# Optimization experiments

Hardware: AMD Instinct MI355X
Metric: run time of the kernel (lower is better)

## Reference

```python
import jax, jax.numpy as jnp
import numpy as np

QS_HIDDEN = 32


def quality_score(feat, W1, b1, W2, b2):
    # (h,5) -> (h,) per-qubit quality in [0,1]
    hdn = jax.nn.relu(feat @ W1 + b1)
    return jax.nn.sigmoid((hdn @ W2 + b2).squeeze(-1))


def _pair_cost(P_log, D, pairs):
    # mean over batch and pairs of sum_{p,q} P_ip * D_pq * P_jq
    Pi = P_log[:, pairs[:, 0], :]  # (batch, E, h)
    Pj = P_log[:, pairs[:, 1], :]  # (batch, E, h)
    return jnp.einsum('beh,hk,bek->be', Pi, D, Pj).mean()


def setup_inputs() -> dict:
    key = jax.random.key(0)
    ks = jax.random.split(key, 10)
    batch, h, L, E = 512, 256, 200, 512
    P = jax.random.uniform(ks[0], (batch, h, h), dtype=jnp.float32)
    P = P / P.sum(-1, keepdims=True)  # row-stochastic (stand-in for doubly stochastic)
    return {
        'P': P,
        'd_error': jax.random.uniform(ks[1], (h, h), dtype=jnp.float32),
        'd_hw': jax.random.uniform(ks[2], (h, h), dtype=jnp.float32),
        'hw_node_features': jax.random.uniform(ks[3], (h, 5), dtype=jnp.float32),
        'qubit_importance': jax.random.uniform(ks[4], (L,), dtype=jnp.float32),
        'W1': jax.random.normal(ks[5], (5, QS_HIDDEN), dtype=jnp.float32) * 0.5,
        'b1': jnp.zeros((QS_HIDDEN,), dtype=jnp.float32),
        'W2': jax.random.normal(ks[6], (QS_HIDDEN, 1), dtype=jnp.float32) * 0.5,
        'b2': jnp.zeros((1,), dtype=jnp.float32),
        'circuit_edge_pairs': jax.random.randint(ks[7], (E, 2), 0, L),
        'cross_circuit_pairs': jax.random.randint(ks[8], (E, 2), 0, L),
        'num_logical': L,
    }


def reference(P, d_error, d_hw, hw_node_features, qubit_importance, W1, b1, W2, b2,
              circuit_edge_pairs, cross_circuit_pairs, num_logical):
    alpha, lambda_sep = 0.3, 0.1
    P_log = P[:, :num_logical, :]  # (batch, L, h)

    # L_surr: error-aware edge loss
    l_surr = _pair_cost(P_log, d_error, circuit_edge_pairs)

    # L_node: node quality loss
    q = quality_score(hw_node_features, W1, b1, W2, b2)  # (h,)
    expected_quality = (P_log * q[None, None, :]).sum(-1)  # (batch, L)
    w_norm = qubit_importance / jnp.clip(qubit_importance.sum(), 1e-8)
    l_node = -(w_norm[None, :] * expected_quality).sum(-1).mean()

    # L_sep: separation loss with max-normalized hardware distance
    d_hw_norm = d_hw / jnp.clip(d_hw.max(), 1e-8)
    l_sep = -_pair_cost(P_log, d_hw_norm, cross_circuit_pairs)

    total = l_surr + alpha * l_node + lambda_sep * l_sep
    return total, l_surr, l_node, l_sep
```

## Files before the change

### kernel.cpp

```cpp
#include <hip/hip_runtime.h>


typedef __attribute__((ext_vector_type(8))) short short8;
typedef __attribute__((ext_vector_type(4))) float float4_;
typedef __attribute__((ext_vector_type(2))) unsigned int uint2_;
typedef __attribute__((ext_vector_type(4))) unsigned int uint4_;

#define HDIM 256
#define LDIM 200

#define WS_DCAT_BYTE_OFF 2048

__device__ __forceinline__ unsigned short f2b(float f) {
  unsigned int u = __float_as_uint(f);
  return (unsigned short)((u + 0x7FFFu + ((u >> 16) & 1u)) >> 16);
}
__device__ __forceinline__ float b2f(unsigned short u) {
  return __uint_as_float(((unsigned int)u) << 16);
}

#if defined(__has_builtin)
#if __has_builtin(__builtin_amdgcn_fdot2_f32_bf16)
#define HAVE_FDOT2 1
#endif
#endif
#ifdef HAVE_FDOT2
typedef __attribute__((ext_vector_type(2))) __bf16 bf16x2;
#endif

__device__ __forceinline__ float dot8acc(uint4_ a, uint4_ b, float acc) {
#ifdef HAVE_FDOT2
#pragma unroll
  for (int d = 0; d < 4; ++d) {
    union { unsigned int u; bf16x2 v; } ua, ub;
    ua.u = a[d]; ub.u = b[d];
    acc = __builtin_amdgcn_fdot2_f32_bf16(ua.v, ub.v, acc, false);
  }
#else
#pragma unroll
  for (int d = 0; d < 4; ++d) {
    float alo = __uint_as_float(a[d] << 16);
    float ahi = __uint_as_float(a[d] & 0xffff0000u);
    float blo = __uint_as_float(b[d] << 16);
    float bhi = __uint_as_float(b[d] & 0xffff0000u);
    acc = fmaf(alo, blo, acc);
    acc = fmaf(ahi, bhi, acc);
  }
#endif
  return acc;
}

__global__ void s2l_prep(const float* __restrict__ feat, const float* __restrict__ W1,
                         const float* __restrict__ bias1, const float* __restrict__ W2,
                         const float* __restrict__ bias2, const float* __restrict__ qi,
                         const float* __restrict__ dhw, float* __restrict__ ws) {
  const int tid = threadIdx.x;
  if (blockIdx.x == 0) {
    __shared__ float red[4];
    float f0 = feat[tid * 5 + 0], f1 = feat[tid * 5 + 1], f2 = feat[tid * 5 + 2];
    float f3 = feat[tid * 5 + 3], f4 = feat[tid * 5 + 4];
    float s = bias2[0];
#pragma unroll
    for (int j = 0; j < 32; ++j) {
      float hd = bias1[j] + f0 * W1[j] + f1 * W1[32 + j] + f2 * W1[64 + j] +
                 f3 * W1[96 + j] + f4 * W1[128 + j];
      s += fmaxf(hd, 0.f) * W2[j];
    }
    ws[16 + tid] = 1.f / (1.f + expf(-s));
    float v = (tid < LDIM) ? qi[tid] : 0.f;
#pragma unroll
    for (int off = 32; off > 0; off >>= 1) v += __shfl_down(v, off);
    if ((tid & 63) == 0) red[tid >> 6] = v;
    __syncthreads();
    if (tid == 0) ws[3] = 1.f / fmaxf(red[0] + red[1] + red[2] + red[3], 1e-8f);
  } else {
    const int idx = (blockIdx.x - 1) * 1024 + tid * 4;
    float4_ v = *(const float4_*)(dhw + idx);
    float m = fmaxf(fmaxf(v[0], v[1]), fmaxf(v[2], v[3]));
#pragma unroll
    for (int off = 32; off > 0; off >>= 1) m = fmaxf(m, __shfl_down(m, off));
    if ((tid & 63) == 0) atomicMax(((unsigned int*)ws) + 5, __float_as_uint(m));
  }
}

__global__ void s2l_dcat(const float* __restrict__ derr, const float* __restrict__ dhw,
                         const float* __restrict__ ws, unsigned short* __restrict__ DcatT) {
  __shared__ float tile[64][65];
  const int ct = blockIdx.x;
  const int ht = blockIdx.y;
  float inv = 1.f;
  if (ct >= 4) {
    float mx = __uint_as_float(((const unsigned int*)ws)[5]);
    inv = 1.f / fmaxf(mx, 1e-8f);
  }
  const float* src = (ct < 4) ? derr : dhw;
  const int c0 = (ct & 3) * 64;
#pragma unroll
  for (int k = 0; k < 16; ++k) {
    int idx = k * 256 + threadIdx.x;
    int lh = idx >> 6, lc = idx & 63;
    tile[lh][lc] = src[(ht * 64 + lh) * 256 + c0 + lc] * inv;
  }
  __syncthreads();
#pragma unroll
  for (int k = 0; k < 16; ++k) {
    int idx = k * 256 + threadIdx.x;
    int lc = idx >> 6, lh = idx & 63;
    DcatT[(size_t)(ct * 64 + lc) * HDIM + ht * 64 + lh] = f2b(tile[lh][lc]);
  }
}

#define P_OFF 0
#define T_OFF 102400
#define TSTRIDE 128
#define TBYTES (208 * TSTRIDE)
#define RED_OFF (T_OFF + 2 * TBYTES)
#define LDS_BYTES (RED_OFF + 64)

__global__ __launch_bounds__(512, 2) void s2l_main(
    const float* __restrict__ P, const int* __restrict__ cpairs,
    const int* __restrict__ xpairs, const float* __restrict__ qi,
    float* __restrict__ ws, const unsigned short* __restrict__ DcatT) {
  __shared__ __attribute__((aligned(16))) unsigned char smem[LDS_BYTES];
  const int tid = threadIdx.x;
  const int wave = tid >> 6, lane = tid & 63;
  const int b = blockIdx.x;
  const int nq = wave >> 1;
  const int mg = wave & 1;
  const int ncol = lane & 15;
  const int kg = lane >> 4;

  const int s0 = (tid & 31) * 8;
  float qreg[8];
#pragma unroll
  for (int e = 0; e < 8; ++e) qreg[e] = ws[16 + s0 + e];
  const float inv_qs = ws[3];

  const float* Pb = P + (size_t)b * (HDIM * HDIM);
  float lnode = 0.f;
  for (int sg = tid; sg < LDIM * 32; sg += 512) {
    int row = sg >> 5, s = sg & 31;
    float4_ a0 = *(const float4_*)(Pb + row * HDIM + s * 8);
    float4_ a1 = *(const float4_*)(Pb + row * HDIM + s * 8 + 4);
    short8 v;
    v[0] = (short)f2b(a0[0]); v[1] = (short)f2b(a0[1]);
    v[2] = (short)f2b(a0[2]); v[3] = (short)f2b(a0[3]);
    v[4] = (short)f2b(a1[0]); v[5] = (short)f2b(a1[1]);
    v[6] = (short)f2b(a1[2]); v[7] = (short)f2b(a1[3]);
    int swz = (s & 24) | ((s & 7) ^ (row & 7));
    *(short8*)(smem + P_OFF + row * 512 + swz * 16) = v;
    float vq = a0[0] * qreg[0] + a0[1] * qreg[1] + a0[2] * qreg[2] + a0[3] * qreg[3] +
               a1[0] * qreg[4] + a1[1] * qreg[5] + a1[2] * qreg[6] + a1[3] * qreg[7];
    lnode += vq * (qi[row] * inv_qs);
  }
  if (tid < 256) {
    int row = 200 + (tid >> 5), s = tid & 31;
    int swz = (s & 24) | ((s & 7) ^ (row & 7));
    *(short8*)(smem + P_OFF + row * 512 + swz * 16) = (short8){0, 0, 0, 0, 0, 0, 0, 0};
  }
  __syncthreads();

  short8 pf[4][8];
#pragma unroll
  for (int nt = 0; nt < 4; ++nt) {
    int prow = (nq * 4 + nt) * 16 + ncol;
#pragma unroll
    for (int ks = 0; ks < 8; ++ks) {
      int slot = ks * 4 + kg;
      int swz = (slot & 24) | ((slot & 7) ^ (prow & 7));
      pf[nt][ks] = *(const short8*)(smem + P_OFF + prow * 512 + swz * 16);
    }
  }

  const int so = tid & 7, p0 = tid >> 3;
  int ip[8], jp[8];
  float s_surr = 0.f, s_sep = 0.f;

#pragma unroll 1
  for (int ct = 0; ct < 8; ++ct) {
    if ((ct & 3) == 0) {
      const int* pr = (ct < 4) ? cpairs : xpairs;
#pragma unroll
      for (int k = 0; k < 8; ++k) {
        int2 pp = *(const int2*)(pr + 2 * (p0 + 64 * k));
        ip[k] = pp.x; jp[k] = pp.y;
      }
    }
    float4_ acc[4][2];
#pragma unroll
    for (int nt = 0; nt < 4; ++nt)
#pragma unroll
      for (int mt = 0; mt < 2; ++mt) acc[nt][mt] = (float4_){0.f, 0.f, 0.f, 0.f};
#pragma unroll
    for (int ks = 0; ks < 8; ++ks) {
      short8 af[2];
#pragma unroll
      for (int mt = 0; mt < 2; ++mt) {
        int c = ct * 64 + mg * 32 + mt * 16 + ncol;
        af[mt] = *(const short8*)(DcatT + c * HDIM + ks * 32 + kg * 8);
      }
#pragma unroll
      for (int nt = 0; nt < 4; ++nt)
#pragma unroll
        for (int mt = 0; mt < 2; ++mt)
          acc[nt][mt] = __builtin_amdgcn_mfma_f32_16x16x32_bf16(af[mt], pf[nt][ks],
                                                                acc[nt][mt], 0, 0, 0);
    }
    unsigned char* Tbuf = smem + T_OFF + (ct & 1) * TBYTES;
#pragma unroll
    for (int nt = 0; nt < 4; ++nt) {
      int prow = (nq * 4 + nt) * 16 + ncol;
#pragma unroll
      for (int mt = 0; mt < 2; ++mt) {
        uint2_ pk;
        pk[0] = (unsigned int)f2b(acc[nt][mt][0]) | ((unsigned int)f2b(acc[nt][mt][1]) << 16);
        pk[1] = (unsigned int)f2b(acc[nt][mt][2]) | ((unsigned int)f2b(acc[nt][mt][3]) << 16);
        int slot = (mg * 32 + mt * 16 + kg * 4) >> 3;
        int off8 = (kg & 1) * 8;
        *(uint2_*)(Tbuf + prow * TSTRIDE + ((slot ^ (prow & 7)) << 4) + off8) = pk;
      }
    }
    __syncthreads();

    float g = 0.f;
#pragma unroll
    for (int k = 0; k < 8; ++k) {
      const int i = ip[k], j = jp[k];
      uint4_ tv = *(const uint4_*)(Tbuf + i * TSTRIDE + ((so ^ (i & 7)) << 4));
      int q = ((ct & 3) * 8) | (so ^ (j & 7));
      uint4_ pv = *(const uint4_*)(smem + P_OFF + j * 512 + (q << 4));
      g = dot8acc(tv, pv, g);
    }
    if (ct < 4) s_surr += g; else s_sep += g;
  }

#pragma unroll
  for (int off = 32; off > 0; off >>= 1) {
    s_surr += __shfl_down(s_surr, off);
    s_sep  += __shfl_down(s_sep, off);
    lnode  += __shfl_down(lnode, off);
  }
  float* red = (float*)(smem + RED_OFF);
  if (lane == 0) { red[wave] = s_surr; red[8 + wave] = s_sep; }
  __syncthreads();
  if (lane == 0 && wave == 0) {
  }
  __syncthreads();
  if (lane == 0) ((float*)(smem + RED_OFF))[0] = red[0];
  if (lane == 0) red[8 + 8 + wave] = lnode;
  __syncthreads();
  if (tid == 0) {
    float a = 0.f, c = 0.f;
    for (int w = 0; w < 8; ++w) { a += red[w]; c += red[8 + w]; }
    atomicAdd(&ws[0], a);
    atomicAdd(&ws[1], c);
  }
  if (lane == 0) atomicAdd(&ws[2], lnode);
}

__global__ void s2l_final(const float* __restrict__ ws, float* __restrict__ out) {
  if (threadIdx.x == 0) {
    const float inv_be = 1.f / (512.f * 512.f);
    float l_surr = ws[0] * inv_be;
    float l_sep = -ws[1] * inv_be;
    float l_node = -ws[2] / 512.f;
    out[0] = l_surr + 0.3f * l_node + 0.1f * l_sep;
    out[1] = l_surr;
    out[2] = l_node;
    out[3] = l_sep;
  }
}

extern "C" void kernel_launch(void* const* d_in, const int* in_sizes, int n_in,
                              void* d_out, int out_size, void* d_ws, size_t ws_size,
                              hipStream_t stream) {
  (void)in_sizes; (void)n_in; (void)out_size; (void)ws_size;
  const float* P     = (const float*)d_in[0];
  const float* d_err = (const float*)d_in[1];
  const float* d_hw  = (const float*)d_in[2];
  const float* feat  = (const float*)d_in[3];
  const float* qi    = (const float*)d_in[4];
  const float* W1    = (const float*)d_in[5];
  const float* bias1 = (const float*)d_in[6];
  const float* W2    = (const float*)d_in[7];
  const float* bias2 = (const float*)d_in[8];
  const int* cpairs  = (const int*)d_in[9];
  const int* xpairs  = (const int*)d_in[10];
  float* ws = (float*)d_ws;
  unsigned short* DcatT = (unsigned short*)((char*)d_ws + WS_DCAT_BYTE_OFF);
  float* out = (float*)d_out;

  hipMemsetAsync(d_ws, 0, 64, stream);
  s2l_prep<<<dim3(65), dim3(256), 0, stream>>>(feat, W1, bias1, W2, bias2, qi, d_hw, ws);
  s2l_dcat<<<dim3(8, 4), dim3(256), 0, stream>>>(d_err, d_hw, ws, DcatT);
  s2l_main<<<dim3(512), dim3(512), 0, stream>>>(P, cpairs, xpairs, qi, ws, DcatT);
  s2l_final<<<dim3(1), dim3(64), 0, stream>>>(ws, out);
}
```

Before: 339.2 us.

## Fuse prep kernels, pre-swizzle D into MFMA fragments, persistent 1024-thread main

Merges the quality-score/max kernel and the D transpose kernel into one launch. D is stored unnormalized as bf16 in MFMA-fragment order, and the 1/max(d_hw) scale is applied to the final sum. The final reduction kernel is replaced by a last-block-done atomic counter inside the main kernel. The main kernel now runs 256 blocks of 1024 threads that each process two batches, with work split across 16 waves. This cuts launch count and makes the D fragment loads contiguous per lane, at the cost of lower occupancy and a serialized P load between the two batches. With the P row padding no longer zeroed, rows 200-207 of shared memory hold stale data. Their MFMA results fill T rows that pair indices (all below 200) should never read.

```diff
diff --git a/kernel.cpp b/kernel.cpp
--- a/kernel.cpp
+++ b/kernel.cpp
@@ -9,14 +9,11 @@
 #define HDIM 256
 #define LDIM 200
 
-#define WS_DCAT_BYTE_OFF 2048
+#define WS_DFRAG_BYTE_OFF 2048
 
 __device__ __forceinline__ unsigned short f2b(float f) {
   unsigned int u = __float_as_uint(f);
   return (unsigned short)((u + 0x7FFFu + ((u >> 16) & 1u)) >> 16);
-}
-__device__ __forceinline__ float b2f(unsigned short u) {
-  return __uint_as_float(((unsigned int)u) << 16);
 }
 
 #if defined(__has_builtin)
@@ -50,10 +47,11 @@
   return acc;
 }
 
-__global__ void s2l_prep(const float* __restrict__ feat, const float* __restrict__ W1,
-                         const float* __restrict__ bias1, const float* __restrict__ W2,
-                         const float* __restrict__ bias2, const float* __restrict__ qi,
-                         const float* __restrict__ dhw, float* __restrict__ ws) {
+__global__ void s2l_pre(const float* __restrict__ feat, const float* __restrict__ W1,
+                        const float* __restrict__ bias1, const float* __restrict__ W2,
+                        const float* __restrict__ bias2, const float* __restrict__ qi,
+                        const float* __restrict__ derr, const float* __restrict__ dhw,
+                        float* __restrict__ ws, unsigned short* __restrict__ Dfrag) {
   const int tid = threadIdx.x;
   if (blockIdx.x == 0) {
     __shared__ float red[4];
@@ -73,40 +71,43 @@
     if ((tid & 63) == 0) red[tid >> 6] = v;
     __syncthreads();
     if (tid == 0) ws[3] = 1.f / fmaxf(red[0] + red[1] + red[2] + red[3], 1e-8f);
-  } else {
-    const int idx = (blockIdx.x - 1) * 1024 + tid * 4;
-    float4_ v = *(const float4_*)(dhw + idx);
-    float m = fmaxf(fmaxf(v[0], v[1]), fmaxf(v[2], v[3]));
+    return;
+  }
+  __shared__ float tile[64][65];
+  const int bid = blockIdx.x - 1;
+  const int c64 = bid >> 2;
+  const int ht = bid & 3;
+  const float* src = (c64 < 4) ? derr : dhw;
+  const int c0 = (c64 & 3) * 64;
+  float m = 0.f;
+#pragma unroll
+  for (int k = 0; k < 16; ++k) {
+    int idx = k * 256 + tid;
+    int lh = idx >> 6, lc = idx & 63;
+    float v = src[(ht * 64 + lh) * 256 + c0 + lc];
+    tile[lh][lc] = v;
+    m = fmaxf(m, v);
+  }
+  if (c64 >= 4) {
 #pragma unroll
     for (int off = 32; off > 0; off >>= 1) m = fmaxf(m, __shfl_down(m, off));
     if ((tid & 63) == 0) atomicMax(((unsigned int*)ws) + 5, __float_as_uint(m));
   }
-}
-
-__global__ void s2l_dcat(const float* __restrict__ derr, const float* __restrict__ dhw,
-                         const float* __restrict__ ws, unsigned short* __restrict__ DcatT) {
-  __shared__ float tile[64][65];
-  const int ct = blockIdx.x;
-  const int ht = blockIdx.y;
-  float inv = 1.f;
-  if (ct >= 4) {
-    float mx = __uint_as_float(((const unsigned int*)ws)[5]);
-    inv = 1.f / fmaxf(mx, 1e-8f);
-  }
-  const float* src = (ct < 4) ? derr : dhw;
-  const int c0 = (ct & 3) * 64;
-#pragma unroll
-  for (int k = 0; k < 16; ++k) {
-    int idx = k * 256 + threadIdx.x;
-    int lh = idx >> 6, lc = idx & 63;
-    tile[lh][lc] = src[(ht * 64 + lh) * 256 + c0 + lc] * inv;
-  }
   __syncthreads();
-#pragma unroll
-  for (int k = 0; k < 16; ++k) {
-    int idx = k * 256 + threadIdx.x;
-    int lc = idx >> 6, lh = idx & 63;
-    DcatT[(size_t)(ct * 64 + lc) * HDIM + ht * 64 + lh] = f2b(tile[lh][lc]);
+  const int lc = tid & 63;
+  const int mg = lc >> 5, mt = (lc >> 4) & 1, ncol = lc & 15;
+#pragma unroll
+  for (int it = 0; it < 2; ++it) {
+    const int g = it * 4 + (tid >> 6);
+    const int h0 = g * 8;
+    const int ks = ht * 2 + (g >> 2);
+    const int kg = g & 3;
+    const int lane = kg * 16 + ncol;
+    short8 v;
+#pragma unroll
+    for (int e = 0; e < 8; ++e) v[e] = (short)f2b(tile[h0 + e][lc]);
+    const int chunk = ((c64 * 2 + mg) * 2 + mt) * 8 + ks;
+    *(short8*)(Dfrag + (size_t)chunk * 512 + lane * 8) = v;
   }
 }
 
@@ -115,123 +116,133 @@
 #define TSTRIDE 128
 #define TBYTES (208 * TSTRIDE)
 #define RED_OFF (T_OFF + 2 * TBYTES)
-#define LDS_BYTES (RED_OFF + 64)
-
-__global__ __launch_bounds__(512, 2) void s2l_main(
+#define LDS_BYTES (RED_OFF + 192)
+
+__global__ __launch_bounds__(1024) void s2l_main(
     const float* __restrict__ P, const int* __restrict__ cpairs,
     const int* __restrict__ xpairs, const float* __restrict__ qi,
-    float* __restrict__ ws, const unsigned short* __restrict__ DcatT) {
+    float* __restrict__ ws, const unsigned short* __restrict__ Dfrag,
+    float* __restrict__ out) {
   __shared__ __attribute__((aligned(16))) unsigned char smem[LDS_BYTES];
   const int tid = threadIdx.x;
   const int wave = tid >> 6, lane = tid & 63;
-  const int b = blockIdx.x;
-  const int nq = wave >> 1;
+  const int ncol = lane & 15, kg = lane >> 4;
+  const int rt0 = wave >> 1;
   const int mg = wave & 1;
-  const int ncol = lane & 15;
-  const int kg = lane >> 4;
-
-  const int s0 = (tid & 31) * 8;
-  float qreg[8];
-#pragma unroll
-  for (int e = 0; e < 8; ++e) qreg[e] = ws[16 + s0 + e];
+  const bool v1 = (rt0 + 8 < 13);
+  const int prow0 = rt0 * 16 + ncol;
+  const int prow1 = (rt0 + 8) * 16 + ncol;
+  const int so = tid & 7, oct = tid >> 3;
   const float inv_qs = ws[3];
 
-  const float* Pb = P + (size_t)b * (HDIM * HDIM);
-  float lnode = 0.f;
-  for (int sg = tid; sg < LDIM * 32; sg += 512) {
-    int row = sg >> 5, s = sg & 31;
-    float4_ a0 = *(const float4_*)(Pb + row * HDIM + s * 8);
-    float4_ a1 = *(const float4_*)(Pb + row * HDIM + s * 8 + 4);
-    short8 v;
-    v[0] = (short)f2b(a0[0]); v[1] = (short)f2b(a0[1]);
-    v[2] = (short)f2b(a0[2]); v[3] = (short)f2b(a0[3]);
-    v[4] = (short)f2b(a1[0]); v[5] = (short)f2b(a1[1]);
-    v[6] = (short)f2b(a1[2]); v[7] = (short)f2b(a1[3]);
-    int swz = (s & 24) | ((s & 7) ^ (row & 7));
-    *(short8*)(smem + P_OFF + row * 512 + swz * 16) = v;
-    float vq = a0[0] * qreg[0] + a0[1] * qreg[1] + a0[2] * qreg[2] + a0[3] * qreg[3] +
-               a1[0] * qreg[4] + a1[1] * qreg[5] + a1[2] * qreg[6] + a1[3] * qreg[7];
-    lnode += vq * (qi[row] * inv_qs);
-  }
-  if (tid < 256) {
-    int row = 200 + (tid >> 5), s = tid & 31;
-    int swz = (s & 24) | ((s & 7) ^ (row & 7));
-    *(short8*)(smem + P_OFF + row * 512 + swz * 16) = (short8){0, 0, 0, 0, 0, 0, 0, 0};
-  }
-  __syncthreads();
-
-  short8 pf[4][8];
-#pragma unroll
-  for (int nt = 0; nt < 4; ++nt) {
-    int prow = (nq * 4 + nt) * 16 + ncol;
+  float s_surr = 0.f, s_sep = 0.f, lnode = 0.f;
+
+#pragma unroll 1
+  for (int bb = 0; bb < 2; ++bb) {
+    const int b = blockIdx.x + bb * 256;
+    const float* Pb = P + (size_t)b * (HDIM * HDIM);
+
+    const int s0q = (tid & 31) * 8;
+    float qreg[8];
+#pragma unroll
+    for (int e = 0; e < 8; ++e) qreg[e] = ws[16 + s0q + e];
+
+    for (int sg = tid; sg < LDIM * 32; sg += 1024) {
+      int row = sg >> 5, s = sg & 31;
+      float4_ a0 = *(const float4_*)(Pb + row * HDIM + s * 8);
+      float4_ a1 = *(const float4_*)(Pb + row * HDIM + s * 8 + 4);
+      short8 v;
+      v[0] = (short)f2b(a0[0]); v[1] = (short)f2b(a0[1]);
+      v[2] = (short)f2b(a0[2]); v[3] = (short)f2b(a0[3]);
+      v[4] = (short)f2b(a1[0]); v[5] = (short)f2b(a1[1]);
+      v[6] = (short)f2b(a1[2]); v[7] = (short)f2b(a1[3]);
+      int swz = (s & 24) | ((s & 7) ^ (row & 7));
+      *(short8*)(smem + P_OFF + row * 512 + swz * 16) = v;
+      float vq = a0[0] * qreg[0] + a0[1] * qreg[1] + a0[2] * qreg[2] + a0[3] * qreg[3] +
+                 a1[0] * qreg[4] + a1[1] * qreg[5] + a1[2] * qreg[6] + a1[3] * qreg[7];
+      lnode += vq * (qi[row] * inv_qs);
+    }
+    __syncthreads();
+
+    short8 pf[2][8];
 #pragma unroll
     for (int ks = 0; ks < 8; ++ks) {
-      int slot = ks * 4 + kg;
-      int swz = (slot & 24) | ((slot & 7) ^ (prow & 7));
-      pf[nt][ks] = *(const short8*)(smem + P_OFF + prow * 512 + swz * 16);
-    }
-  }
-
-  const int so = tid & 7, p0 = tid >> 3;
-  int ip[8], jp[8];
-  float s_surr = 0.f, s_sep = 0.f;
-
+      {
+        int slot = ks * 4 + kg;
+        int swz = (slot & 24) | ((slot & 7) ^ (prow0 & 7));
+        pf[0][ks] = *(const short8*)(smem + P_OFF + prow0 * 512 + swz * 16);
+      }
+      {
+        int slot = ks * 4 + kg;
+        int swz = (slot & 24) | ((slot & 7) ^ (prow1 & 7));
+        pf[1][ks] = *(const short8*)(smem + P_OFF + prow1 * 512 + swz * 16);
+      }
+    }
+
+    int ip[4], jp[4];
 #pragma unroll 1
-  for (int ct = 0; ct < 8; ++ct) {
-    if ((ct & 3) == 0) {
-      const int* pr = (ct < 4) ? cpairs : xpairs;
-#pragma unroll
-      for (int k = 0; k < 8; ++k) {
-        int2 pp = *(const int2*)(pr + 2 * (p0 + 64 * k));
-        ip[k] = pp.x; jp[k] = pp.y;
-      }
-    }
-    float4_ acc[4][2];
-#pragma unroll
-    for (int nt = 0; nt < 4; ++nt)
-#pragma unroll
-      for (int mt = 0; mt < 2; ++mt) acc[nt][mt] = (float4_){0.f, 0.f, 0.f, 0.f};
-#pragma unroll
-    for (int ks = 0; ks < 8; ++ks) {
-      short8 af[2];
-#pragma unroll
-      for (int mt = 0; mt < 2; ++mt) {
-        int c = ct * 64 + mg * 32 + mt * 16 + ncol;
-        af[mt] = *(const short8*)(DcatT + c * HDIM + ks * 32 + kg * 8);
-      }
-#pragma unroll
-      for (int nt = 0; nt < 4; ++nt)
+    for (int ct = 0; ct < 8; ++ct) {
+      if ((ct & 3) == 0) {
+        const int* pr = (ct < 4) ? cpairs : xpairs;
+#pragma unroll
+        for (int k = 0; k < 4; ++k) {
+          int2 pp = *(const int2*)(pr + 2 * (oct + 128 * k));
+          ip[k] = pp.x; jp[k] = pp.y;
+        }
+      }
+      float4_ acc[2][2];
+#pragma unroll
+      for (int nt = 0; nt < 2; ++nt)
+#pragma unroll
+        for (int mt = 0; mt < 2; ++mt) acc[nt][mt] = (float4_){0.f, 0.f, 0.f, 0.f};
+#pragma unroll
+      for (int ks = 0; ks < 8; ++ks) {
+        short8 af[2];
+#pragma unroll
+        for (int mt = 0; mt < 2; ++mt) {
+          const int chunk = ((ct * 2 + mg) * 2 + mt) * 8 + ks;
+          af[mt] = *(const short8*)(Dfrag + (size_t)chunk * 512 + lane * 8);
+        }
 #pragma unroll
         for (int mt = 0; mt < 2; ++mt)
-          acc[nt][mt] = __builtin_amdgcn_mfma_f32_16x16x32_bf16(af[mt], pf[nt][ks],
-                                                                acc[nt][mt], 0, 0, 0);
-    }
-    unsigned char* Tbuf = smem + T_OFF + (ct & 1) * TBYTES;
-#pragma unroll
-    for (int nt = 0; nt < 4; ++nt) {
-      int prow = (nq * 4 + nt) * 16 + ncol;
-#pragma unroll
-      for (int mt = 0; mt < 2; ++mt) {
-        uint2_ pk;
-        pk[0] = (unsigned int)f2b(acc[nt][mt][0]) | ((unsigned int)f2b(acc[nt][mt][1]) << 16);
-        pk[1] = (unsigned int)f2b(acc[nt][mt][2]) | ((unsigned int)f2b(acc[nt][mt][3]) << 16);
-        int slot = (mg * 32 + mt * 16 + kg * 4) >> 3;
-        int off8 = (kg & 1) * 8;
-        *(uint2_*)(Tbuf + prow * TSTRIDE + ((slot ^ (prow & 7)) << 4) + off8) = pk;
-      }
+          acc[0][mt] = __builtin_amdgcn_mfma_f32_16x16x32_bf16(af[mt], pf[0][ks],
+                                                               acc[0][mt], 0, 0, 0);
+        if (v1) {
+#pragma unroll
+          for (int mt = 0; mt < 2; ++mt)
+            acc[1][mt] = __builtin_amdgcn_mfma_f32_16x16x32_bf16(af[mt], pf[1][ks],
+                                                                 acc[1][mt], 0, 0, 0);
+        }
+      }
+      unsigned char* Tbuf = smem + T_OFF + (ct & 1) * TBYTES;
+#pragma unroll
+      for (int nt = 0; nt < 2; ++nt) {
+        if (nt == 1 && !v1) break;
+        const int prow = nt ? prow1 : prow0;
+#pragma unroll
+        for (int mt = 0; mt < 2; ++mt) {
+          uint2_ pk;
+          pk[0] = (unsigned int)f2b(acc[nt][mt][0]) | ((unsigned int)f2b(acc[nt][mt][1]) << 16);
+          pk[1] = (unsigned int)f2b(acc[nt][mt][2]) | ((unsigned int)f2b(acc[nt][mt][3]) << 16);
+          const int slot = (mg * 32 + mt * 16 + kg * 4) >> 3;
+          const int off8 = (kg & 1) * 8;
+          *(uint2_*)(Tbuf + prow * TSTRIDE + ((slot ^ (prow & 7)) << 4) + off8) = pk;
+        }
+      }
+      __syncthreads();
+
+      float g = 0.f;
+#pragma unroll
+      for (int k = 0; k < 4; ++k) {
+        const int i = ip[k], j = jp[k];
+        uint4_ tv = *(const uint4_*)(Tbuf + i * TSTRIDE + ((so ^ (i & 7)) << 4));
+        const int q = ((ct & 3) * 8) | (so ^ (j & 7));
+        uint4_ pv = *(const uint4_*)(smem + P_OFF + j * 512 + (q << 4));
+        g = dot8acc(tv, pv, g);
+      }
+      if (ct < 4) s_surr += g; else s_sep += g;
     }
     __syncthreads();
-
-    float g = 0.f;
-#pragma unroll
-    for (int k = 0; k < 8; ++k) {
-      const int i = ip[k], j = jp[k];
-      uint4_ tv = *(const uint4_*)(Tbuf + i * TSTRIDE + ((so ^ (i & 7)) << 4));
-      int q = ((ct & 3) * 8) | (so ^ (j & 7));
-      uint4_ pv = *(const uint4_*)(smem + P_OFF + j * 512 + (q << 4));
-      g = dot8acc(tv, pv, g);
-    }
-    if (ct < 4) s_surr += g; else s_sep += g;
   }
 
 #pragma unroll
@@ -241,33 +252,30 @@
     lnode  += __shfl_down(lnode, off);
   }
   float* red = (float*)(smem + RED_OFF);
-  if (lane == 0) { red[wave] = s_surr; red[8 + wave] = s_sep; }
-  __syncthreads();
-  if (lane == 0 && wave == 0) {
-  }
-  __syncthreads();
-  if (lane == 0) ((float*)(smem + RED_OFF))[0] = red[0];
-  if (lane == 0) red[8 + 8 + wave] = lnode;
+  if (lane == 0) { red[wave] = s_surr; red[16 + wave] = s_sep; red[32 + wave] = lnode; }
   __syncthreads();
   if (tid == 0) {
-    float a = 0.f, c = 0.f;
-    for (int w = 0; w < 8; ++w) { a += red[w]; c += red[8 + w]; }
+    float a = 0.f, c = 0.f, l = 0.f;
+    for (int w = 0; w < 16; ++w) { a += red[w]; c += red[16 + w]; l += red[32 + w]; }
     atomicAdd(&ws[0], a);
     atomicAdd(&ws[1], c);
-  }
-  if (lane == 0) atomicAdd(&ws[2], lnode);
-}
-
-__global__ void s2l_final(const float* __restrict__ ws, float* __restrict__ out) {
-  if (threadIdx.x == 0) {
-    const float inv_be = 1.f / (512.f * 512.f);
-    float l_surr = ws[0] * inv_be;
-    float l_sep = -ws[1] * inv_be;
-    float l_node = -ws[2] / 512.f;
-    out[0] = l_surr + 0.3f * l_node + 0.1f * l_sep;
-    out[1] = l_surr;
-    out[2] = l_node;
-    out[3] = l_sep;
+    atomicAdd(&ws[2], l);
+    __threadfence();
+    unsigned int done = atomicAdd(((unsigned int*)ws) + 6, 1u);
+    if (done == 255u) {
+      float S_surr = atomicAdd(&ws[0], 0.f);
+      float S_sep  = atomicAdd(&ws[1], 0.f);
+      float S_node = atomicAdd(&ws[2], 0.f);
+      float mx = __uint_as_float(((unsigned int*)ws)[5]);
+      const float inv_be = 1.f / (512.f * 512.f);
+      float l_surr = S_surr * inv_be;
+      float l_sep = -(S_sep * inv_be) / fmaxf(mx, 1e-8f);
+      float l_node = -S_node / 512.f;
+      out[0] = l_surr + 0.3f * l_node + 0.1f * l_sep;
+      out[1] = l_surr;
+      out[2] = l_node;
+      out[3] = l_sep;
+    }
   }
 }
 
@@ -287,12 +295,11 @@
   const int* cpairs  = (const int*)d_in[9];
   const int* xpairs  = (const int*)d_in[10];
   float* ws = (float*)d_ws;
-  unsigned short* DcatT = (unsigned short*)((char*)d_ws + WS_DCAT_BYTE_OFF);
+  unsigned short* Dfrag = (unsigned short*)((char*)d_ws + WS_DFRAG_BYTE_OFF);
   float* out = (float*)d_out;
 
   hipMemsetAsync(d_ws, 0, 64, stream);
-  s2l_prep<<<dim3(65), dim3(256), 0, stream>>>(feat, W1, bias1, W2, bias2, qi, d_hw, ws);
-  s2l_dcat<<<dim3(8, 4), dim3(256), 0, stream>>>(d_err, d_hw, ws, DcatT);
-  s2l_main<<<dim3(512), dim3(512), 0, stream>>>(P, cpairs, xpairs, qi, ws, DcatT);
-  s2l_final<<<dim3(1), dim3(64), 0, stream>>>(ws, out);
-}
+  s2l_pre<<<dim3(33), dim3(256), 0, stream>>>(feat, W1, bias1, W2, bias2, qi,
+                                              d_err, d_hw, ws, Dfrag);
+  s2l_main<<<dim3(256), dim3(1024), 0, stream>>>(P, cpairs, xpairs, qi, ws, Dfrag, out);
+}
```

After: 275.5 us. 18.8% less time.
